# Kernel optimization log

Measured on AMD Instinct MI355X. Metric: run time of the kernel, lower is better.

## Reference

```python
import jax, jax.numpy as jnp
import numpy as np

N, E = 50000, 400000
F_IN, HID, OUT, H = 128, 64, 40, 4
SLOPE = 0.2


def setup_inputs() -> dict:
    key = jax.random.key(0)
    ks = jax.random.split(key, 20)

    def gn(k, shape, scale=0.05):
        return jax.random.normal(k, shape, dtype=jnp.float32) * scale

    inp = {
        "node_inputs": jax.random.normal(ks[0], (N, F_IN), dtype=jnp.float32),
        "src": jax.random.randint(ks[1], (E,), 0, N),
        "dst": jax.random.randint(ks[2], (E,), 0, N),
    }
    # (in_dim, per-head out_dim) per layer; residual linear only when in != heads*out
    dims = [(F_IN, HID), (H * HID, HID), (H * HID, OUT)]
    i = 3
    for l, (fin, d) in enumerate(dims):
        inp[f"w_src{l}"] = gn(ks[i], (fin, H * d)); i += 1
        inp[f"b_src{l}"] = jnp.zeros((H * d,), jnp.float32)
        inp[f"w_dst{l}"] = gn(ks[i], (fin, H * d)); i += 1
        inp[f"b_dst{l}"] = jnp.zeros((H * d,), jnp.float32)
        inp[f"attn{l}"] = gn(ks[i], (H, d)); i += 1
        if fin != H * d:
            inp[f"w_res{l}"] = gn(ks[i], (fin, H * d)); i += 1
            inp[f"b_res{l}"] = jnp.zeros((H * d,), jnp.float32)
    return inp


def _gatv2_layer(x, src, dst, w_s, b_s, w_d, b_d, attn, res):
    # x: [N, F]; res: [N, H*D] residual term (already projected or identity)
    n = x.shape[0]
    h, d = attn.shape
    hs = (x @ w_s + b_s).reshape(n, h, d)   # feat_src
    hd = (x @ w_d + b_d).reshape(n, h, d)   # feat_dst
    e = hs[src] + hd[dst]                    # [E, H, D]
    e = jnp.where(e > 0, e, SLOPE * e)       # LeakyReLU
    logits = jnp.einsum('ehd,hd->eh', e, attn)  # [E, H]
    # edge softmax over incoming edges of each dst node
    m = jax.ops.segment_max(logits, dst, num_segments=n)
    z = jnp.exp(logits - m[dst])
    s = jax.ops.segment_sum(z, dst, num_segments=n)
    a = z / s[dst]                            # [E, H]
    out = jax.ops.segment_sum(hs[src] * a[:, :, None], dst, num_segments=n)  # [N, H, D]
    return out + res.reshape(n, h, d)


def reference(node_inputs, src, dst,
              w_src0, b_src0, w_dst0, b_dst0, attn0, w_res0, b_res0,
              w_src1, b_src1, w_dst1, b_dst1, attn1,
              w_src2, b_src2, w_dst2, b_dst2, attn2, w_res2, b_res2):
    x = node_inputs
    # layer 0: in=128 != heads*hid -> linear residual
    x = _gatv2_layer(x, src, dst, w_src0, b_src0, w_dst0, b_dst0, attn0,
                     x @ w_res0 + b_res0)
    x = x.reshape(x.shape[0], -1)  # flatten heads
    # layer 1: in == heads*hid -> identity residual
    x = _gatv2_layer(x, src, dst, w_src1, b_src1, w_dst1, b_dst1, attn1, x)
    x = x.reshape(x.shape[0], -1)
    # layer 2: in=256 != heads*out -> linear residual
    x = _gatv2_layer(x, src, dst, w_src2, b_src2, w_dst2, b_dst2, attn2,
                     x @ w_res2 + b_res2)
    # mean over heads: [N, H, OUT] -> [N, OUT]
    return x.mean(axis=-2)
```

## Files before the change

### kernel.cpp

```cpp
#include <hip/hip_runtime.h>
#include <hip/hip_bf16.h>
#include <math.h>

#define SLOPE 0.2f

typedef unsigned short bf16_t;
typedef short bh8 __attribute__((ext_vector_type(8)));
typedef unsigned short us8 __attribute__((ext_vector_type(8)));
typedef float f32x4 __attribute__((ext_vector_type(4)));

__device__ __forceinline__ float bf2f(bf16_t x) {
    return __uint_as_float((unsigned)x << 16);
}
__device__ __forceinline__ bf16_t f2bf(float v) {
    unsigned u = __float_as_uint(v);
    return (bf16_t)((u + 0x7FFFu + ((u >> 16) & 1u)) >> 16);
}
__device__ __forceinline__ ushort2 pk_f2bf(float a, float b) {
    __hip_bfloat162 h2 = __float22bfloat162_rn(float2{a, b});
    union { __hip_bfloat162 h; ushort2 u; } u;
    u.h = h2;
    return u.u;
}


__global__ void hist_and_convert(
    const int* __restrict__ dst, int E, int eblocks, int* __restrict__ deg,
    const float* __restrict__ w0, const float* __restrict__ w1, const float* __restrict__ w2,
    const float* __restrict__ w3, const float* __restrict__ w4,
    const float* __restrict__ w5, const float* __restrict__ w6,
    const float* __restrict__ wr2, const float* __restrict__ br2,
    bf16_t* __restrict__ t0, bf16_t* __restrict__ t1, bf16_t* __restrict__ t2,
    bf16_t* __restrict__ t3, bf16_t* __restrict__ t4,
    bf16_t* __restrict__ t5, bf16_t* __restrict__ t6,
    bf16_t* __restrict__ teff, float* __restrict__ b_eff)
{
    int t = threadIdx.x;
    if ((int)blockIdx.x < eblocks) {
        int e = blockIdx.x * 256 + t;
        if (e < E) atomicAdd(&deg[dst[e]], 1);
        return;
    }
    int b = blockIdx.x - eblocks;
    const float* W; bf16_t* T; int K, Nc, lb;
    if (b < 384) {
        int g = b / 128; lb = b - g * 128;
        W = g == 0 ? w0 : (g == 1 ? w1 : w2);
        T = g == 0 ? t0 : (g == 1 ? t1 : t2);
        K = 128; Nc = 256;
    } else if (b < 896) {
        int g = (b - 384) / 256; lb = (b - 384) - g * 256;
        W = g == 0 ? w3 : w4; T = g == 0 ? t3 : t4;
        K = 256; Nc = 256;
    } else if (b < 1280) {
        int g = (b - 896) / 192; lb = (b - 896) - g * 192;
        W = g == 0 ? w5 : w6; T = g == 0 ? t5 : t6;
        K = 256; Nc = 160;
    } else {
        lb = b - 1280;
        int idx = lb * 256 + t;
        int n = idx >> 8, k = idx & 255;
        float v = 0.f;
        if (n < 40)
            v = 0.25f * (wr2[(size_t)k * 160 + n] + wr2[(size_t)k * 160 + 40 + n] +
                         wr2[(size_t)k * 160 + 80 + n] + wr2[(size_t)k * 160 + 120 + n]);
        teff[idx] = f2bf(v);
        if (lb == 0 && t < 40)
            b_eff[t] = 0.25f * (br2[t] + br2[40 + t] + br2[80 + t] + br2[120 + t]);
        return;
    }
    int idx = lb * 256 + t;
    int n = idx / K, k = idx - n * K;
    float v = (n < Nc) ? W[(size_t)k * Nc + n] : 0.f;
    T[idx] = f2bf(v);
}


__global__ void deg_chunk_sum(const int* __restrict__ deg, int n,
                              int* __restrict__ chunk_sums, int* __restrict__ bcnt) {
    __shared__ int sm[256];
    __shared__ int hl[128];
    int t = threadIdx.x;
    if (t < 128) hl[t] = 0;
    __syncthreads();
    int base = blockIdx.x * 1024;
    int s = 0;
    for (int i = t; i < 1024; i += 256) {
        int idx = base + i;
        if (idx < n) {
            int d = deg[idx];
            s += d;
            atomicAdd(&hl[d < 127 ? d : 127], 1);
        }
    }
    sm[t] = s;
    __syncthreads();
    for (int off = 128; off > 0; off >>= 1) {
        if (t < off) sm[t] += sm[t + off];
        __syncthreads();
    }
    if (t == 0) chunk_sums[blockIdx.x] = sm[0];
    if (t < 128 && hl[t]) atomicAdd(&bcnt[t], hl[t]);
}

__global__ void scan_write(const int* __restrict__ deg, int n,
                           const int* __restrict__ chunk_sums,
                           int* __restrict__ row_start, int Etot,
                           const int* __restrict__ bcnt, int* __restrict__ bfill,
                           int* __restrict__ perm) {
    __shared__ int sm[256];
    __shared__ int s_pref;
    __shared__ int sbase[128];
    __shared__ int lcnt[128];
    __shared__ int gbase[128];
    int base = blockIdx.x * 1024;
    int t = threadIdx.x;

    if (t < 128) lcnt[t] = 0;

    if (t < 64) {
        int v = (t < (int)blockIdx.x) ? chunk_sums[t] : 0;
#pragma unroll
        for (int off = 32; off > 0; off >>= 1)
            v += __shfl_down(v, off, 64);
        if (t == 0) s_pref = v;
    }
    if (t == 128) {
        int run = 0;
        for (int i = 0; i < 128; i++) { sbase[i] = run; run += bcnt[i]; }
    }

    int vv[4];
    int tsum = 0;
#pragma unroll
    for (int j = 0; j < 4; j++) {
        int idx = base + t * 4 + j;
        vv[j] = (idx < n) ? deg[idx] : 0;
        tsum += vv[j];
    }
    sm[t] = tsum;
    __syncthreads();
    for (int off = 1; off < 256; off <<= 1) {
        int x = (t >= off) ? sm[t - off] : 0;
        __syncthreads();
        sm[t] += x;
        __syncthreads();
    }
    int excl = sm[t] - tsum + s_pref;
#pragma unroll
    for (int j = 0; j < 4; j++) {
        int idx = base + t * 4 + j;
        if (idx < n) row_start[idx] = excl;
        excl += vv[j];
    }
    if (blockIdx.x == 0 && t == 0) row_start[n] = Etot;

    int rnk[4], bb[4];
#pragma unroll
    for (int j = 0; j < 4; j++) {
        int idx = base + t * 4 + j;
        if (idx < n) {
            bb[j] = vv[j] < 127 ? vv[j] : 127;
            rnk[j] = atomicAdd(&lcnt[bb[j]], 1);
        } else bb[j] = -1;
    }
    __syncthreads();
    if (t < 128 && lcnt[t]) gbase[t] = atomicAdd(&bfill[t], lcnt[t]);
    __syncthreads();
#pragma unroll
    for (int j = 0; j < 4; j++) {
        int idx = base + t * 4 + j;
        if (bb[j] >= 0)
            perm[sbase[bb[j]] + gbase[bb[j]] + rnk[j]] = idx;
    }
}


template <typename TA, int NOUT, int KTOT, int NPAD, bool SPLIT40, bool HAS_EFF, bool DO_SCATTER>
__global__ __launch_bounds__(256) void gemm_lds(
    const TA* __restrict__ A,
    const bf16_t* __restrict__ Wt0, const bf16_t* __restrict__ Wt1, const bf16_t* __restrict__ Wt2,
    const float* __restrict__ bias0, const float* __restrict__ bias1, const float* __restrict__ bias2,
    bf16_t* __restrict__ C0, bf16_t* __restrict__ C1, bf16_t* __restrict__ C2,
    const bf16_t* __restrict__ Wte, const float* __restrict__ biase, float* __restrict__ Ce,
    int M, int Nc,
    const int* __restrict__ e_dst, const int* __restrict__ e_src, int E,
    const int* __restrict__ row_start, int* __restrict__ fill,
    int* __restrict__ src_sorted, int mtiles)
{
    constexpr int LSTR = KTOT + 8;
    constexpr int ESTR = 38;
    constexpr int KC = KTOT / 32;
    __shared__ bf16_t As[64 * LSTR];
    __shared__ bf16_t Ep[4 * 64 * ESTR];

    int tid = threadIdx.x;

    if (DO_SCATTER && (int)blockIdx.x >= mtiles) {
        int e = (blockIdx.x - mtiles) * 256 + tid;
        if (e < E) {
            int d_ = e_dst[e];
            int pos = row_start[d_] + atomicAdd(&fill[d_], 1);
            src_sorted[pos] = e_src[e];
        }
        return;
    }

    int lane = tid & 63, w = tid >> 6;
    int lm = lane & 15, lq = lane >> 4;
    int m0 = blockIdx.x * 64;

    const bf16_t* Wts[3] = {Wt0, Wt1, Wt2};
    const float* biases[3] = {bias0, bias1, bias2};
    bf16_t* Cs[3] = {C0, C1, C2};

    if (sizeof(TA) == 4) {
#pragma unroll
        for (int it = 0; it < 4; it++) {
            int idx = tid + it * 256;
            int r = idx >> 4, c = idx & 15;
            int gm = m0 + r; if (gm >= M) gm = M - 1;
            const float* ap = (const float*)A + (size_t)gm * KTOT + c * 8;
            float4 lo = *(const float4*)ap;
            float4 hi = *(const float4*)(ap + 4);
            ushort2 p0 = pk_f2bf(lo.x, lo.y), p1 = pk_f2bf(lo.z, lo.w);
            ushort2 p2 = pk_f2bf(hi.x, hi.y), p3 = pk_f2bf(hi.z, hi.w);
            bh8 v = { (short)p0.x, (short)p0.y, (short)p1.x, (short)p1.y,
                      (short)p2.x, (short)p2.y, (short)p3.x, (short)p3.y };
            *(bh8*)(As + r * LSTR + c * 8) = v;
        }
    } else {
#pragma unroll
        for (int it = 0; it < 8; it++) {
            int idx = tid + it * 256;
            int r = idx >> 5, c = idx & 31;
            int gm = m0 + r; if (gm >= M) gm = M - 1;
            bh8 v = *(const bh8*)((const bf16_t*)A + (size_t)gm * KTOT + c * 8);
            *(bh8*)(As + r * LSTR + c * 8) = v;
        }
    }
    __syncthreads();

    bf16_t* ep = Ep + w * (64 * ESTR);
    constexpr int NCHUNK = (NPAD + 127) / 128;

#pragma unroll
    for (int chunk = 0; chunk < NCHUNK; chunk++) {
        int n0 = chunk * 128 + w * 32;
        if (n0 >= NPAD) continue;

        int boff[NOUT][2];
#pragma unroll
        for (int o = 0; o < NOUT; o++)
#pragma unroll
            for (int nt = 0; nt < 2; nt++)
                boff[o][nt] = (n0 + nt * 16 + lm) * KTOT + lq * 8;

        f32x4 acc[NOUT][4][2];
#pragma unroll
        for (int o = 0; o < NOUT; o++)
#pragma unroll
            for (int i = 0; i < 4; i++)
#pragma unroll
                for (int j = 0; j < 2; j++)
                    acc[o][i][j] = (f32x4){0.f, 0.f, 0.f, 0.f};

        bh8 bf_cur[NOUT][2], bf_nxt[NOUT][2];
#pragma unroll
        for (int o = 0; o < NOUT; o++)
#pragma unroll
            for (int nt = 0; nt < 2; nt++)
                bf_cur[o][nt] = *(const bh8*)(Wts[o] + boff[o][nt]);

#pragma unroll
        for (int kc = 0; kc < KC; kc++) {
            if (kc + 1 < KC) {
#pragma unroll
                for (int o = 0; o < NOUT; o++)
#pragma unroll
                    for (int nt = 0; nt < 2; nt++)
                        bf_nxt[o][nt] = *(const bh8*)(Wts[o] + boff[o][nt] + (kc + 1) * 32);
            }
            bh8 af[4];
#pragma unroll
            for (int mt = 0; mt < 4; mt++)
                af[mt] = *(const bh8*)(As + (mt * 16 + lm) * LSTR + kc * 32 + lq * 8);
#pragma unroll
            for (int o = 0; o < NOUT; o++)
#pragma unroll
                for (int mt = 0; mt < 4; mt++)
#pragma unroll
                    for (int nt = 0; nt < 2; nt++)
                        acc[o][mt][nt] = __builtin_amdgcn_mfma_f32_16x16x32_bf16(af[mt], bf_cur[o][nt], acc[o][mt][nt], 0, 0, 0);
            if (kc + 1 < KC) {
#pragma unroll
                for (int o = 0; o < NOUT; o++)
#pragma unroll
                    for (int nt = 0; nt < 2; nt++)
                        bf_cur[o][nt] = bf_nxt[o][nt];
            }
        }

#pragma unroll
        for (int o = 0; o < NOUT; o++) {
#pragma unroll
            for (int nt = 0; nt < 2; nt++) {
                int gn = n0 + nt * 16 + lm;
                float bv = (gn < Nc) ? biases[o][gn] : 0.f;
#pragma unroll
                for (int mt = 0; mt < 4; mt++)
#pragma unroll
                    for (int r = 0; r < 4; r++)
                        ep[(mt * 16 + lq * 4 + r) * ESTR + nt * 16 + lm] = f2bf(acc[o][mt][nt][r] + bv);
            }
#pragma unroll
            for (int it = 0; it < 4; it++) {
                int row = it * 16 + (lane >> 2);
                int cc = (lane & 3) * 8;
                bh8 v = *(const bh8*)(ep + row * ESTR + cc);
                int gm = m0 + row;
                int cg = n0 + cc;
                if (gm < M && cg < Nc) {
                    size_t cb = SPLIT40 ? (size_t)(cg + 24 * (cg / 40)) : (size_t)cg;
                    size_t rs = SPLIT40 ? 256 : (size_t)Nc;
                    *(bh8*)(Cs[o] + (size_t)gm * rs + cb) = v;
                }
            }
        }
    }

    if (HAS_EFF && w < 2) {
        int beoff[2];
#pragma unroll
        for (int nt = 0; nt < 2; nt++)
            beoff[nt] = (w * 32 + nt * 16 + lm) * KTOT + lq * 8;
        f32x4 acc_e[4][2];
#pragma unroll
        for (int i = 0; i < 4; i++)
#pragma unroll
            for (int j = 0; j < 2; j++)
                acc_e[i][j] = (f32x4){0.f, 0.f, 0.f, 0.f};
#pragma unroll
        for (int kc = 0; kc < KC; kc++) {
            bh8 af[4];
#pragma unroll
            for (int mt = 0; mt < 4; mt++)
                af[mt] = *(const bh8*)(As + (mt * 16 + lm) * LSTR + kc * 32 + lq * 8);
            bh8 be[2];
#pragma unroll
            for (int nt = 0; nt < 2; nt++)
                be[nt] = *(const bh8*)(Wte + beoff[nt] + kc * 32);
#pragma unroll
            for (int mt = 0; mt < 4; mt++)
#pragma unroll
                for (int nt = 0; nt < 2; nt++)
                    acc_e[mt][nt] = __builtin_amdgcn_mfma_f32_16x16x32_bf16(af[mt], be[nt], acc_e[mt][nt], 0, 0, 0);
        }
#pragma unroll
        for (int nt = 0; nt < 2; nt++) {
            int gn = w * 32 + nt * 16 + lm;
            if (gn >= 40) continue;
            float bv = biase[gn];
#pragma unroll
            for (int mt = 0; mt < 4; mt++)
#pragma unroll
                for (int r = 0; r < 4; r++) {
                    int gm = m0 + mt * 16 + lq * 4 + r;
                    if (gm < M) Ce[(size_t)gm * 40 + gn] = acc_e[mt][nt][r] + bv;
                }
        }
    }
}


__device__ __forceinline__ void us8_to_f(const us8 v, float* h) {
#pragma unroll
    for (int j = 0; j < 8; j++) h[j] = bf2f(v[j]);
}

__device__ __forceinline__ float edge_logit16(const float h[16], const float hdf[16], const float at[16]) {
    float p = 0.f;
#pragma unroll
    for (int j = 0; j < 16; j++) {
        float q = h[j] + hdf[j];
        p += fmaxf(q, SLOPE * q) * at[j];
    }
    p += __shfl_xor(p, 1, 64);
    p += __shfl_xor(p, 2, 64);
    return p;
}

template <int DVALID, bool FINAL, bool RES_INPLACE>
__global__ __launch_bounds__(256) void gat_agg_quarter(
    const bf16_t* __restrict__ hs, const bf16_t* __restrict__ hd,
    const float* __restrict__ attn,
    const int* __restrict__ row_start, const int* __restrict__ src_sorted,
    const int* __restrict__ perm,
    bf16_t* __restrict__ P, float* __restrict__ out_final, int N)
{
    int w = threadIdx.x >> 6, lane = threadIdx.x & 63;
    int q = lane >> 4, ql = lane & 15;
    int gq = blockIdx.x * 16 + w * 4 + q;
    if (gq >= N) return;
    int n = perm[gq];
    int f0 = ql * 16;
    int h = ql >> 2;
    int dp = (ql & 3) * 16;

    float at[16], hdf[16];
#pragma unroll
    for (int j = 0; j < 16; j++)
        at[j] = (dp + j < DVALID) ? attn[h * DVALID + dp + j] : 0.f;
    {
        us8 a = *(const us8*)(hd + (unsigned)(n * 256 + f0));
        us8 b = *(const us8*)(hd + (unsigned)(n * 256 + f0 + 8));
        us8_to_f(a, hdf); us8_to_f(b, hdf + 8);
    }

    float pc;
    {
        float p = 0.f;
#pragma unroll
        for (int j = 0; j < 16; j++) {
            float qq = hdf[j];
            p += fmaxf(qq, SLOPE * qq) * at[j];
        }
        p += __shfl_xor(p, 1, 64);
        p += __shfl_xor(p, 2, 64);
        pc = p;
    }

    int s = row_start[n], e = row_start[n + 1];

    float cl0 = 0.f, cl1 = 0.f;
    float ca0[16] = {}, ca1[16] = {};

    int i = s;
    for (; i + 2 <= e; i += 2) {
        int sn0 = src_sorted[i], sn1 = src_sorted[i + 1];
        us8 r0a = *(const us8*)(hs + (unsigned)(sn0 * 256 + f0));
        us8 r0b = *(const us8*)(hs + (unsigned)(sn0 * 256 + f0 + 8));
        us8 r1a = *(const us8*)(hs + (unsigned)(sn1 * 256 + f0));
        us8 r1b = *(const us8*)(hs + (unsigned)(sn1 * 256 + f0 + 8));
        float h0[16], h1[16];
        us8_to_f(r0a, h0); us8_to_f(r0b, h0 + 8);
        us8_to_f(r1a, h1); us8_to_f(r1b, h1 + 8);
        float w0 = __expf(edge_logit16(h0, hdf, at) - pc);
        float w1 = __expf(edge_logit16(h1, hdf, at) - pc);
        cl0 += w0; cl1 += w1;
#pragma unroll
        for (int j = 0; j < 16; j++) {
            ca0[j] += w0 * h0[j];
            ca1[j] += w1 * h1[j];
        }
    }
    if (i < e) {
        int sn0 = src_sorted[i];
        us8 r0a = *(const us8*)(hs + (unsigned)(sn0 * 256 + f0));
        us8 r0b = *(const us8*)(hs + (unsigned)(sn0 * 256 + f0 + 8));
        float h0[16];
        us8_to_f(r0a, h0); us8_to_f(r0b, h0 + 8);
        float w0 = __expf(edge_logit16(h0, hdf, at) - pc);
        cl0 += w0;
#pragma unroll
        for (int j = 0; j < 16; j++) ca0[j] += w0 * h0[j];
    }

    float v[16] = {};
    if (e > s) {
        float inv = 1.f / (cl0 + cl1);
#pragma unroll
        for (int j = 0; j < 16; j++)
            v[j] = (ca0[j] + ca1[j]) * inv;
    }

    if (FINAL) {
#pragma unroll
        for (int j = 0; j < 16; j++) {
            v[j] += __shfl_xor(v[j], 4, 64);
            v[j] += __shfl_xor(v[j], 8, 64);
        }
        if (h == 0) {
#pragma unroll
            for (int jj = 0; jj < 16; jj += 4) {
                if (dp + jj < DVALID) {
                    float* op = out_final + (unsigned)(n * DVALID + dp + jj);
                    float4 cur = *(float4*)op;
                    cur.x += 0.25f * v[jj];
                    cur.y += 0.25f * v[jj + 1];
                    cur.z += 0.25f * v[jj + 2];
                    cur.w += 0.25f * v[jj + 3];
                    *(float4*)op = cur;
                }
            }
        }
    } else {
        unsigned oi = (unsigned)(n * 256 + f0);
        if (RES_INPLACE) {
            us8 pa = *(const us8*)(P + oi);
            us8 pb = *(const us8*)(P + oi + 8);
#pragma unroll
            for (int j = 0; j < 8; j++) {
                v[j] += bf2f(pa[j]);
                v[8 + j] += bf2f(pb[j]);
            }
        }
        us8 oa, ob;
#pragma unroll
        for (int j = 0; j < 8; j++) {
            oa[j] = f2bf(v[j]);
            ob[j] = f2bf(v[8 + j]);
        }
        *(us8*)(P + oi) = oa;
        *(us8*)(P + oi + 8) = ob;
    }
}


extern "C" void kernel_launch(void* const* d_in, const int* in_sizes, int n_in,
                              void* d_out, int out_size, void* d_ws, size_t ws_size,
                              hipStream_t stream) {
    const float* x0    = (const float*)d_in[0];
    const int*   src   = (const int*)d_in[1];
    const int*   dst   = (const int*)d_in[2];
    const float* w_src0 = (const float*)d_in[3];  const float* b_src0 = (const float*)d_in[4];
    const float* w_dst0 = (const float*)d_in[5];  const float* b_dst0 = (const float*)d_in[6];
    const float* attn0  = (const float*)d_in[7];
    const float* w_res0 = (const float*)d_in[8];  const float* b_res0 = (const float*)d_in[9];
    const float* w_src1 = (const float*)d_in[10]; const float* b_src1 = (const float*)d_in[11];
    const float* w_dst1 = (const float*)d_in[12]; const float* b_dst1 = (const float*)d_in[13];
    const float* attn1  = (const float*)d_in[14];
    const float* w_src2 = (const float*)d_in[15]; const float* b_src2 = (const float*)d_in[16];
    const float* w_dst2 = (const float*)d_in[17]; const float* b_dst2 = (const float*)d_in[18];
    const float* attn2  = (const float*)d_in[19];
    const float* w_res2 = (const float*)d_in[20]; const float* b_res2 = (const float*)d_in[21];

    const int N = in_sizes[0] / 128;
    const int E = in_sizes[1];
    float* out = (float*)d_out;
    (void)n_in; (void)out_size; (void)ws_size;

    char* ws = (char*)d_ws;
    size_t off = 0;
    auto alloc = [&](size_t bytes) {
        void* q = ws + off;
        off = (off + bytes + 255) & ~(size_t)255;
        return q;
    };
    int* deg        = (int*)alloc((size_t)2 * N * 4);
    int* fill       = deg + N;
    int* bcnt       = (int*)alloc(256 * 4);
    int* bfill      = bcnt + 128;
    int* perm       = (int*)alloc((size_t)N * 4);
    int* row_start  = (int*)alloc((size_t)(N + 1) * 4);
    int* chunk_sums = (int*)alloc(256 * 4);
    int* src_sorted = (int*)alloc((size_t)E * 4);
    bf16_t* t_src0 = (bf16_t*)alloc(256 * 128 * 2);
    bf16_t* t_dst0 = (bf16_t*)alloc(256 * 128 * 2);
    bf16_t* t_res0 = (bf16_t*)alloc(256 * 128 * 2);
    bf16_t* t_src1 = (bf16_t*)alloc(256 * 256 * 2);
    bf16_t* t_dst1 = (bf16_t*)alloc(256 * 256 * 2);
    bf16_t* t_src2 = (bf16_t*)alloc(192 * 256 * 2);
    bf16_t* t_dst2 = (bf16_t*)alloc(192 * 256 * 2);
    bf16_t* t_eff  = (bf16_t*)alloc(64 * 256 * 2);
    float*  b_eff  = (float*)alloc(64 * 4);
    const size_t elems = (size_t)N * 256;
    bf16_t* P  = (bf16_t*)alloc(elems * 2);
    bf16_t* HS = (bf16_t*)alloc(elems * 2);
    bf16_t* HD = (bf16_t*)alloc(elems * 2);

    hipMemsetAsync(deg, 0, (size_t)2 * N * 4, stream);
    hipMemsetAsync(bcnt, 0, 256 * 4, stream);
    int eblocks = (E + 255) / 256;
    int nchunks = (N + 1023) / 1024;
    hipLaunchKernelGGL(hist_and_convert, dim3(eblocks + 1344), dim3(256), 0, stream,
                       dst, E, eblocks, deg,
                       w_src0, w_dst0, w_res0, w_src1, w_dst1, w_src2, w_dst2, w_res2, b_res2,
                       t_src0, t_dst0, t_res0, t_src1, t_dst1, t_src2, t_dst2, t_eff, b_eff);
    hipLaunchKernelGGL(deg_chunk_sum, dim3(nchunks), dim3(256), 0, stream, deg, N, chunk_sums, bcnt);
    hipLaunchKernelGGL(scan_write, dim3(nchunks), dim3(256), 0, stream, deg, N, chunk_sums,
                       row_start, E, bcnt, bfill, perm);

    dim3 blk(256);
    int mtiles = (N + 63) / 64;
    int ab = (N + 15) / 16;

    hipLaunchKernelGGL((gemm_lds<float, 3, 128, 256, false, false, true>),
                       dim3(mtiles + eblocks), blk, 0, stream,
                       x0, t_src0, t_dst0, t_res0, b_src0, b_dst0, b_res0,
                       HS, HD, P,
                       (const bf16_t*)nullptr, (const float*)nullptr, (float*)nullptr,
                       N, 256,
                       dst, src, E, row_start, fill, src_sorted, mtiles);
    hipLaunchKernelGGL((gat_agg_quarter<64, false, true>), dim3(ab), blk, 0, stream,
                       HS, HD, attn0, row_start, src_sorted, perm, P, (float*)nullptr, N);

    hipLaunchKernelGGL((gemm_lds<bf16_t, 2, 256, 256, false, false, false>), dim3(mtiles), blk, 0, stream,
                       P, t_src1, t_dst1, (const bf16_t*)nullptr, b_src1, b_dst1, (const float*)nullptr,
                       HS, HD, (bf16_t*)nullptr,
                       (const bf16_t*)nullptr, (const float*)nullptr, (float*)nullptr,
                       N, 256,
                       (const int*)nullptr, (const int*)nullptr, 0,
                       (const int*)nullptr, (int*)nullptr, (int*)nullptr, 0);
    hipLaunchKernelGGL((gat_agg_quarter<64, false, true>), dim3(ab), blk, 0, stream,
                       HS, HD, attn1, row_start, src_sorted, perm, P, (float*)nullptr, N);

    hipLaunchKernelGGL((gemm_lds<bf16_t, 2, 256, 192, true, true, false>), dim3(mtiles), blk, 0, stream,
                       P, t_src2, t_dst2, (const bf16_t*)nullptr, b_src2, b_dst2, (const float*)nullptr,
                       HS, HD, (bf16_t*)nullptr,
                       t_eff, b_eff, out,
                       N, 160,
                       (const int*)nullptr, (const int*)nullptr, 0,
                       (const int*)nullptr, (int*)nullptr, (int*)nullptr, 0);
    hipLaunchKernelGGL((gat_agg_quarter<40, true, false>), dim3(ab), blk, 0, stream,
                       HS, HD, attn2, row_start, src_sorted, perm, (bf16_t*)nullptr, out, N);
}
```

Before: 415.0 us.

## Software-pipeline edge gathers in GAT aggregation with reversed node order

Restructures the per-destination edge loop into a software pipeline that prefetches the next four source rows (and their indices) while the current four are processed, with a single accumulator set instead of two. It also sets a launch-bounds occupancy hint of 4 and walks the degree-sorted permutation in reverse order, so heavier nodes are likely scheduled first. The goal is to hide gather latency and reduce tail imbalance. The prefetch buffers raise register pressure and could clash with the occupancy hint.

Measured after the change: 597.1 us. 43.9% more time.

```diff
diff --git a/kernel.cpp b/kernel.cpp
--- a/kernel.cpp
+++ b/kernel.cpp
@@ -378,20 +378,8 @@
     for (int j = 0; j < 8; j++) h[j] = bf2f(v[j]);
 }
 
-__device__ __forceinline__ float edge_logit16(const float h[16], const float hdf[16], const float at[16]) {
-    float p = 0.f;
-#pragma unroll
-    for (int j = 0; j < 16; j++) {
-        float q = h[j] + hdf[j];
-        p += fmaxf(q, SLOPE * q) * at[j];
-    }
-    p += __shfl_xor(p, 1, 64);
-    p += __shfl_xor(p, 2, 64);
-    return p;
-}
-
 template <int DVALID, bool FINAL, bool RES_INPLACE>
-__global__ __launch_bounds__(256) void gat_agg_quarter(
+__global__ __launch_bounds__(256, 4) void gat_agg_quarter(
     const bf16_t* __restrict__ hs, const bf16_t* __restrict__ hd,
     const float* __restrict__ attn,
     const int* __restrict__ row_start, const int* __restrict__ src_sorted,
@@ -402,7 +390,7 @@
     int q = lane >> 4, ql = lane & 15;
     int gq = blockIdx.x * 16 + w * 4 + q;
     if (gq >= N) return;
-    int n = perm[gq];
+    int n = perm[(N - 1) - gq];
     int f0 = ql * 16;
     int h = ql >> 2;
     int dp = (ql & 3) * 16;
@@ -432,46 +420,74 @@
 
     int s = row_start[n], e = row_start[n + 1];
 
-    float cl0 = 0.f, cl1 = 0.f;
-    float ca0[16] = {}, ca1[16] = {};
+    float cl = 0.f;
+    float ca[16] = {};
+
+    auto proc = [&](const us8 ra, const us8 rb) {
+        float p = 0.f;
+#pragma unroll
+        for (int j = 0; j < 8; j++) {
+            float qa = bf2f(ra[j]) + hdf[j];
+            p += fmaxf(qa, SLOPE * qa) * at[j];
+            float qb = bf2f(rb[j]) + hdf[8 + j];
+            p += fmaxf(qb, SLOPE * qb) * at[8 + j];
+        }
+        p += __shfl_xor(p, 1, 64);
+        p += __shfl_xor(p, 2, 64);
+        float wk = __expf(p - pc);
+        cl += wk;
+#pragma unroll
+        for (int j = 0; j < 8; j++) {
+            ca[j]     += wk * bf2f(ra[j]);
+            ca[8 + j] += wk * bf2f(rb[j]);
+        }
+    };
+
+#define GA(sn) (*(const us8*)(hs + (unsigned)((sn) * 256 + f0)))
+#define GB(sn) (*(const us8*)(hs + (unsigned)((sn) * 256 + f0 + 8)))
 
     int i = s;
+    if (i + 8 <= e) {
+        int a0 = src_sorted[i], a1 = src_sorted[i + 1];
+        int a2 = src_sorted[i + 2], a3 = src_sorted[i + 3];
+        us8 c0a = GA(a0), c0b = GB(a0), c1a = GA(a1), c1b = GB(a1);
+        us8 c2a = GA(a2), c2b = GB(a2), c3a = GA(a3), c3b = GB(a3);
+        int b0 = src_sorted[i + 4], b1 = src_sorted[i + 5];
+        int b2 = src_sorted[i + 6], b3 = src_sorted[i + 7];
+
+        for (; i + 8 <= e; i += 4) {
+            us8 n0a = GA(b0), n0b = GB(b0), n1a = GA(b1), n1b = GB(b1);
+            us8 n2a = GA(b2), n2b = GB(b2), n3a = GA(b3), n3b = GB(b3);
+            if (i + 12 <= e) {
+                b0 = src_sorted[i + 8];  b1 = src_sorted[i + 9];
+                b2 = src_sorted[i + 10]; b3 = src_sorted[i + 11];
+            }
+            proc(c0a, c0b); proc(c1a, c1b); proc(c2a, c2b); proc(c3a, c3b);
+            c0a = n0a; c0b = n0b; c1a = n1a; c1b = n1b;
+            c2a = n2a; c2b = n2b; c3a = n3a; c3b = n3b;
+        }
+        proc(c0a, c0b); proc(c1a, c1b); proc(c2a, c2b); proc(c3a, c3b);
+        i += 4;
+    }
     for (; i + 2 <= e; i += 2) {
-        int sn0 = src_sorted[i], sn1 = src_sorted[i + 1];
-        us8 r0a = *(const us8*)(hs + (unsigned)(sn0 * 256 + f0));
-        us8 r0b = *(const us8*)(hs + (unsigned)(sn0 * 256 + f0 + 8));
-        us8 r1a = *(const us8*)(hs + (unsigned)(sn1 * 256 + f0));
-        us8 r1b = *(const us8*)(hs + (unsigned)(sn1 * 256 + f0 + 8));
-        float h0[16], h1[16];
-        us8_to_f(r0a, h0); us8_to_f(r0b, h0 + 8);
-        us8_to_f(r1a, h1); us8_to_f(r1b, h1 + 8);
-        float w0 = __expf(edge_logit16(h0, hdf, at) - pc);
-        float w1 = __expf(edge_logit16(h1, hdf, at) - pc);
-        cl0 += w0; cl1 += w1;
-#pragma unroll
-        for (int j = 0; j < 16; j++) {
-            ca0[j] += w0 * h0[j];
-            ca1[j] += w1 * h1[j];
-        }
+        int a0 = src_sorted[i], a1 = src_sorted[i + 1];
+        us8 r0a = GA(a0), r0b = GB(a0), r1a = GA(a1), r1b = GB(a1);
+        proc(r0a, r0b); proc(r1a, r1b);
     }
     if (i < e) {
-        int sn0 = src_sorted[i];
-        us8 r0a = *(const us8*)(hs + (unsigned)(sn0 * 256 + f0));
-        us8 r0b = *(const us8*)(hs + (unsigned)(sn0 * 256 + f0 + 8));
-        float h0[16];
-        us8_to_f(r0a, h0); us8_to_f(r0b, h0 + 8);
-        float w0 = __expf(edge_logit16(h0, hdf, at) - pc);
-        cl0 += w0;
-#pragma unroll
-        for (int j = 0; j < 16; j++) ca0[j] += w0 * h0[j];
-    }
+        int a0 = src_sorted[i];
+        us8 r0a = GA(a0), r0b = GB(a0);
+        proc(r0a, r0b);
+    }
+#undef GA
+#undef GB
 
     float v[16] = {};
     if (e > s) {
-        float inv = 1.f / (cl0 + cl1);
+        float inv = 1.f / cl;
 #pragma unroll
         for (int j = 0; j < 16; j++)
-            v[j] = (ca0[j] + ca1[j]) * inv;
+            v[j] = ca[j] * inv;
     }
 
     if (FINAL) {
```
